# Optimization experiments

Hardware: AMD Instinct MI355X
Metric: run time of the kernel (lower is better)

Reference implementation:

```python
import jax, jax.numpy as jnp
import numpy as np

B, T, D, NH = 2, 2048, 2048, 16
HID = D  # hidden_dim must equal emb_dim for the source's fc2(x1) to type-check
HD = D // NH
EPS = 1e-5


def setup_inputs() -> dict:
    key = jax.random.key(0)
    ks = jax.random.split(key, 16)
    s = 0.02
    inp = {
        "x": jax.random.normal(ks[0], (B, T, D), jnp.float32),
        "Wq": jax.random.normal(ks[1], (D, D), jnp.float32) * s,
        "bq": jnp.zeros((D,), jnp.float32),
        "Wk": jax.random.normal(ks[2], (D, D), jnp.float32) * s,
        "bk": jnp.zeros((D,), jnp.float32),
        "Wv": jax.random.normal(ks[3], (D, D), jnp.float32) * s,
        "bv": jnp.zeros((D,), jnp.float32),
        "Wo": jax.random.normal(ks[4], (D, D), jnp.float32) * s,
        "bo": jnp.zeros((D,), jnp.float32),
        "scale1": jnp.ones((D,), jnp.float32),
        "scale2": jnp.ones((D,), jnp.float32),
        "W1": jax.random.normal(ks[5], (D, HID), jnp.float32) * s,
        "W2": jax.random.normal(ks[6], (D, HID), jnp.float32) * s,  # fc2: Linear(emb_dim, hidden_dim)
        "W3": jax.random.normal(ks[7], (HID, D), jnp.float32) * s,
    }
    return inp


def _rmsnorm(x, scale):
    m = jnp.mean(x * x, axis=-1, keepdims=True)
    return scale * (x * jax.lax.rsqrt(m + EPS))


def _attention(x, Wq, bq, Wk, bk, Wv, bv, Wo, bo):
    b, t, _ = x.shape
    q = (x @ Wq + bq).reshape(b, t, NH, HD)
    k = (x @ Wk + bk).reshape(b, t, NH, HD)
    v = (x @ Wv + bv).reshape(b, t, NH, HD)
    # energy: [B, H, T, T]; softmax over keys, scaled by 1/sqrt(head_dim); NO causal mask in source
    energy = jnp.einsum("bqhd,bkhd->bhqk", q, k) / jnp.sqrt(jnp.float32(HD))
    attn = jax.nn.softmax(energy, axis=-1)
    out = jnp.einsum("bhqk,bkhd->bqhd", attn, v).reshape(b, t, D)
    return out @ Wo + bo


def _ffn(x, W1, W2, W3):
    x1 = x @ W1                       # [B,T,HID]
    x2 = x1 @ W2                      # source quirk: fc2 applied to x1 (hidden_dim == emb_dim)
    return (x1 * jax.nn.sigmoid(x1) * x2) @ W3


def reference(x, Wq, bq, Wk, bk, Wv, bv, Wo, bo, scale1, scale2, W1, W2, W3):
    shortcut = x
    h = _rmsnorm(x, scale1)
    h = _attention(h, Wq, bq, Wk, bk, Wv, bv, Wo, bo)
    h = shortcut + h
    h = _rmsnorm(h, scale2)
    h = _ffn(h, W1, W2, W3)
    # source adds the ORIGINAL input again (shortcut never reassigned)
    return h + shortcut
```

## Files before the change

kernel.cpp:

```cpp
#include <hip/hip_runtime.h>

typedef __bf16 bf16x8 __attribute__((ext_vector_type(8)));
typedef __bf16 bf16x4v __attribute__((ext_vector_type(4)));
typedef float  f32x4  __attribute__((ext_vector_type(4)));

#define LDS_AS(p) ((__attribute__((address_space(3))) void*)(p))
#define GLB_AS(p) ((const __attribute__((address_space(1))) void*)(p))

#define QSCL (0.08838834764831845f * 1.4426950408889634f)

struct TP { const float* s[7]; __bf16* d[7]; float sc[7]; };
__global__ __launch_bounds__(256) void transpose_convert_all(TP p) {
  const float* __restrict__ W = p.s[blockIdx.z];
  __bf16* __restrict__ Wt = p.d[blockIdx.z];
  const float sc = p.sc[blockIdx.z];
  __shared__ float tile[32][33];
  const int tx = threadIdx.x & 31, ty = threadIdx.x >> 5;
  const int n0 = blockIdx.x * 32, k0 = blockIdx.y * 32;
#pragma unroll
  for (int j = 0; j < 4; ++j)
    tile[ty + j * 8][tx] = W[(size_t)(k0 + ty + j * 8) * 2048 + n0 + tx];
  __syncthreads();
#pragma unroll
  for (int j = 0; j < 4; ++j)
    Wt[(size_t)(n0 + ty + j * 8) * 2048 + k0 + tx] = (__bf16)(tile[tx][ty + j * 8] * sc);
}

__global__ __launch_bounds__(256) void rmsnorm_k(
    const float* __restrict__ x, const float* __restrict__ scale,
    __bf16* __restrict__ out) {
  const int row = blockIdx.x, t = threadIdx.x;
  const float4* xr = (const float4*)(x + (size_t)row * 2048);
  float4 a = xr[t], b2 = xr[t + 256];
  float ss = a.x * a.x + a.y * a.y + a.z * a.z + a.w * a.w +
             b2.x * b2.x + b2.y * b2.y + b2.z * b2.z + b2.w * b2.w;
#pragma unroll
  for (int ofs = 32; ofs; ofs >>= 1) ss += __shfl_xor(ss, ofs, 64);
  __shared__ float red[4];
  if ((t & 63) == 0) red[t >> 6] = ss;
  __syncthreads();
  ss = red[0] + red[1] + red[2] + red[3];
  const float rs = rsqrtf(ss * (1.f / 2048.f) + 1e-5f);
  const float4* sr = (const float4*)scale;
  float4 s1 = sr[t], s2 = sr[t + 256];
  __bf16* orow = out + (size_t)row * 2048;
  orow[t * 4 + 0] = (__bf16)(a.x * rs * s1.x);
  orow[t * 4 + 1] = (__bf16)(a.y * rs * s1.y);
  orow[t * 4 + 2] = (__bf16)(a.z * rs * s1.z);
  orow[t * 4 + 3] = (__bf16)(a.w * rs * s1.w);
  orow[(t + 256) * 4 + 0] = (__bf16)(b2.x * rs * s2.x);
  orow[(t + 256) * 4 + 1] = (__bf16)(b2.y * rs * s2.y);
  orow[(t + 256) * 4 + 2] = (__bf16)(b2.z * rs * s2.z);
  orow[(t + 256) * 4 + 3] = (__bf16)(b2.w * rs * s2.w);
}

template <bool OUTF32, bool HASBIAS, bool HASRES, bool SILU, bool VTRANS = false>
__global__ __launch_bounds__(256) void gemm_bt(
    const __bf16* __restrict__ A, const __bf16* __restrict__ Bt,
    const float* __restrict__ bias, const float* __restrict__ res,
    const __bf16* __restrict__ ew, void* __restrict__ Cout,
    int M, int N, int Kd) {
  __shared__ __attribute__((aligned(16))) __bf16 As[2][128 * 32];
  __shared__ __attribute__((aligned(16))) __bf16 Bs[2][128 * 32];
  const int tid = threadIdx.x;
  const int w = tid >> 6, l = tid & 63;
  const int flat = blockIdx.y * gridDim.x + blockIdx.x;
  const int nwg = gridDim.x * gridDim.y;
  const int swz = (flat & 7) * (nwg >> 3) + (flat >> 3);
  const int bx = swz % gridDim.x, by = swz / gridDim.x;
  const int M0 = by * 128, N0 = bx * 128;
  const int wr = w >> 1, wc = w & 1;
  const int lm = l & 15, lq = l >> 4;

  f32x4 acc[4][4];
#pragma unroll
  for (int mt = 0; mt < 4; ++mt)
#pragma unroll
    for (int nt = 0; nt < 4; ++nt)
#pragma unroll
      for (int e = 0; e < 4; ++e) acc[mt][nt][e] = 0.f;

  const int offA0 = (w * 2 + 0) * 1024 + l * 16;
  const int offA1 = (w * 2 + 1) * 1024 + l * 16;
  const int row0 = offA0 >> 6, kb0 = offA0 & 63;
  const int row1 = offA1 >> 6, kb1 = offA1 & 63;
  const int nIt = Kd >> 5;

  auto stage = [&](int k0, int bsel) {
    const char* ga0 = (const char*)(A + (size_t)(M0 + row0) * Kd + k0) + kb0;
    const char* ga1 = (const char*)(A + (size_t)(M0 + row1) * Kd + k0) + kb1;
    const char* gb0 = (const char*)(Bt + (size_t)(N0 + row0) * Kd + k0) + kb0;
    const char* gb1 = (const char*)(Bt + (size_t)(N0 + row1) * Kd + k0) + kb1;
    __builtin_amdgcn_global_load_lds(GLB_AS(ga0), LDS_AS(((char*)As[bsel]) + (w * 2 + 0) * 1024), 16, 0, 0);
    __builtin_amdgcn_global_load_lds(GLB_AS(ga1), LDS_AS(((char*)As[bsel]) + (w * 2 + 1) * 1024), 16, 0, 0);
    __builtin_amdgcn_global_load_lds(GLB_AS(gb0), LDS_AS(((char*)Bs[bsel]) + (w * 2 + 0) * 1024), 16, 0, 0);
    __builtin_amdgcn_global_load_lds(GLB_AS(gb1), LDS_AS(((char*)Bs[bsel]) + (w * 2 + 1) * 1024), 16, 0, 0);
  };

  stage(0, 0);
  for (int it = 0; it < nIt; ++it) {
    __syncthreads();
    if (it + 1 < nIt) stage((it + 1) * 32, (it + 1) & 1);
    const __bf16* Ab = As[it & 1];
    const __bf16* Bb = Bs[it & 1];
    bf16x8 af[4], bfr[4];
#pragma unroll
    for (int mt = 0; mt < 4; ++mt)
      af[mt] = *(const bf16x8*)(Ab + (wr * 64 + mt * 16 + lm) * 32 + lq * 8);
#pragma unroll
    for (int nt = 0; nt < 4; ++nt)
      bfr[nt] = *(const bf16x8*)(Bb + (wc * 64 + nt * 16 + lm) * 32 + lq * 8);
#pragma unroll
    for (int mt = 0; mt < 4; ++mt)
#pragma unroll
      for (int nt = 0; nt < 4; ++nt)
        acc[mt][nt] = __builtin_amdgcn_mfma_f32_16x16x32_bf16(af[mt], bfr[nt], acc[mt][nt], 0, 0, 0);
  }

  const int lr = lq * 4;
#pragma unroll
  for (int mt = 0; mt < 4; ++mt) {
#pragma unroll
    for (int nt = 0; nt < 4; ++nt) {
      const int col = N0 + wc * 64 + nt * 16 + lm;
      float bv = 0.f;
      if (HASBIAS) bv = bias[col];
      if (VTRANS) {
        const int rw0 = M0 + wr * 64 + mt * 16 + lr;
        const int bidx = rw0 >> 11, tok = rw0 & 2047;
        bf16x4v pk;
#pragma unroll
        for (int i = 0; i < 4; ++i) pk[i] = (__bf16)(acc[mt][nt][i] + bv);
        *(bf16x4v*)((__bf16*)Cout + ((size_t)(bidx * 2048 + col)) * 2048 + tok) = pk;
      } else {
#pragma unroll
        for (int i = 0; i < 4; ++i) {
          const int row = M0 + wr * 64 + mt * 16 + lr + i;
          const size_t off = (size_t)row * N + col;
          float v = acc[mt][nt][i] + bv;
          if (HASRES) v += res[off];
          if (SILU) {
            const float x1v = (float)ew[off];
            v = x1v * (1.f / (1.f + __expf(-x1v))) * v;
          }
          if (OUTF32) ((float*)Cout)[off] = v;
          else ((__bf16*)Cout)[off] = (__bf16)v;
        }
      }
    }
  }
}

__global__ __launch_bounds__(512, 2) void gemm_qkv(
    const __bf16* __restrict__ A, const __bf16* __restrict__ Bt,
    const float* __restrict__ bq, const float* __restrict__ bk,
    __bf16* __restrict__ Qout, __bf16* __restrict__ Kout, int Kd) {
  __shared__ __attribute__((aligned(16))) char lds[2][4][16384];

  const int tid = threadIdx.x;
  const int w = tid >> 6, l = tid & 63;
  const int wr = w >> 2, wc = w & 3;
  const int lm = l & 15, lq = l >> 4;

  const int flat = blockIdx.y * 16 + blockIdx.x;
  const int swz = (flat & 7) * 32 + (flat >> 3);
  const int bx = swz >> 4, by = swz & 15;
  const int N0 = bx * 256, M0 = by * 256;

  const int srow = w * 8 + (l >> 3);
  const int scol = ((l & 7) ^ (l >> 3)) * 8;
  const __bf16* aS = A + (size_t)(M0 + srow) * Kd + scol;
  const __bf16* bS = Bt + (size_t)(N0 + srow) * Kd + scol;

  auto stageHT = [&](int t, int s, int db) {
    char* dst = lds[db][s] + w * 1024;
    const __bf16* src = (s >= 2) ? (aS + (size_t)(s - 2) * 128 * Kd + t * 64)
                                 : (bS + (size_t)s * 128 * Kd + t * 64);
    __builtin_amdgcn_global_load_lds(GLB_AS(src), LDS_AS(dst), 16, 0, 0);
    __builtin_amdgcn_global_load_lds(GLB_AS(src + (size_t)64 * Kd), LDS_AS(dst + 8192), 16, 0, 0);
  };

  f32x4 acc[8][4];
#pragma unroll
  for (int m = 0; m < 8; ++m)
#pragma unroll
    for (int n = 0; n < 4; ++n)
#pragma unroll
      for (int e = 0; e < 4; ++e) acc[m][n][e] = 0.f;

  const int swzr = (lm & 7) << 4;
  const int c0 = (lq * 16) ^ swzr;
  const int c1 = ((64 + lq * 16)) ^ swzr;
  const int arow = lm * 128;
  const int brow = ((wc & 1) * 64 + lm) * 128;

  stageHT(0, 0, 0); stageHT(0, 1, 0); stageHT(0, 2, 0); stageHT(0, 3, 0);
  stageHT(1, 0, 1); stageHT(1, 1, 1); stageHT(1, 2, 1);
  asm volatile("s_waitcnt vmcnt(6)" ::: "memory");
  __builtin_amdgcn_s_barrier();

  const int NT = Kd >> 6;
  bf16x8 af[4][2], bfr[4][2];

#define BAR()                                            \
  do {                                                   \
    asm volatile("" ::: "memory");                       \
    __builtin_amdgcn_s_barrier();                        \
    asm volatile("" ::: "memory");                       \
  } while (0)

#define MFMA_QUAD(MB, NB)                                                          \
  do {                                                                             \
    _Pragma("unroll") for (int m = 0; m < 4; ++m)                                  \
      _Pragma("unroll") for (int n = 0; n < 2; ++n) {                              \
        acc[(MB) + m][(NB) + n] = __builtin_amdgcn_mfma_f32_16x16x32_bf16(         \
            af[m][0], bfr[(NB) + n][0], acc[(MB) + m][(NB) + n], 0, 0, 0);         \
        acc[(MB) + m][(NB) + n] = __builtin_amdgcn_mfma_f32_16x16x32_bf16(         \
            af[m][1], bfr[(NB) + n][1], acc[(MB) + m][(NB) + n], 0, 0, 0);         \
      }                                                                            \
  } while (0)

#define TILE_BODY(T, BUF)                                                       \
  do {                                                                          \
    const char* Ab = lds[BUF][2 + wr];                                          \
    const char* Bb = lds[BUF][wc >> 1];                                         \
    _Pragma("unroll") for (int m = 0; m < 4; ++m) {                             \
      af[m][0] = *(const bf16x8*)(Ab + arow + m * 2048 + c0);                   \
      af[m][1] = *(const bf16x8*)(Ab + arow + m * 2048 + c1);                   \
    }                                                                           \
    _Pragma("unroll") for (int n = 0; n < 4; ++n) {                             \
      bfr[n][0] = *(const bf16x8*)(Bb + brow + n * 2048 + c0);                  \
      bfr[n][1] = *(const bf16x8*)(Bb + brow + n * 2048 + c1);                  \
    }                                                                           \
    if ((T) + 1 < NT) stageHT((T) + 1, 3, (BUF) ^ 1);                           \
    BAR();                                                                      \
    __builtin_amdgcn_s_setprio(1);                                              \
    MFMA_QUAD(0, 0);                                                            \
    __builtin_amdgcn_s_setprio(0);                                              \
    asm volatile("s_waitcnt lgkmcnt(0)" ::: "memory");                          \
    BAR();                                                                      \
    if ((T) + 2 < NT) stageHT((T) + 2, 0, BUF);                                 \
    BAR();                                                                      \
    __builtin_amdgcn_s_setprio(1);                                              \
    MFMA_QUAD(0, 2);                                                            \
    __builtin_amdgcn_s_setprio(0);                                              \
    BAR();                                                                      \
    _Pragma("unroll") for (int m = 0; m < 4; ++m) {                             \
      af[m][0] = *(const bf16x8*)(Ab + arow + (m + 4) * 2048 + c0);             \
      af[m][1] = *(const bf16x8*)(Ab + arow + (m + 4) * 2048 + c1);             \
    }                                                                           \
    if ((T) + 2 < NT) stageHT((T) + 2, 1, BUF);                                 \
    BAR();                                                                      \
    __builtin_amdgcn_s_setprio(1);                                              \
    MFMA_QUAD(4, 0);                                                            \
    __builtin_amdgcn_s_setprio(0);                                              \
    asm volatile("s_waitcnt lgkmcnt(0)" ::: "memory");                          \
    BAR();                                                                      \
    if ((T) + 2 < NT) stageHT((T) + 2, 2, BUF);                                 \
    BAR();                                                                      \
    __builtin_amdgcn_s_setprio(1);                                              \
    MFMA_QUAD(4, 2);                                                            \
    __builtin_amdgcn_s_setprio(0);                                              \
    if ((T) + 2 < NT) { asm volatile("s_waitcnt vmcnt(6)" ::: "memory"); }      \
    else { asm volatile("s_waitcnt vmcnt(0)" ::: "memory"); }                   \
    BAR();                                                                      \
  } while (0)

  for (int tp = 0; tp < NT; tp += 2) {
    TILE_BODY(tp, 0);
    TILE_BODY(tp + 1, 1);
  }
#undef TILE_BODY
#undef MFMA_QUAD
#undef BAR

  const int seg = N0 >> 11;
  const int nbase = N0 & 2047;
  const float* bb = (seg == 0) ? bq : bk;
  const float bsc = (seg == 0) ? QSCL : 1.f;
  __bf16* dst = (seg == 0) ? Qout : Kout;
#pragma unroll
  for (int m = 0; m < 8; ++m) {
#pragma unroll
    for (int n = 0; n < 4; ++n) {
      const int col = nbase + wc * 64 + n * 16 + lm;
      const float bvv = bb[col] * bsc;
#pragma unroll
      for (int i = 0; i < 4; ++i) {
        const int row = M0 + wr * 128 + m * 16 + lq * 4 + i;
        dst[(size_t)row * 2048 + col] = (__bf16)(acc[m][n][i] + bvv);
      }
    }
  }
}

__global__ __launch_bounds__(256, 2) void attn_mfma(
    const __bf16* __restrict__ Q, const __bf16* __restrict__ K,
    const __bf16* __restrict__ Vt, __bf16* __restrict__ O) {
  __shared__ __attribute__((aligned(16))) char KsL[2][16 * 1024];
  __shared__ __attribute__((aligned(16))) char VsL[2][16 * 1024];

  const int t = threadIdx.x;
  const int w = t >> 6, l = t & 63;
  const int lm = l & 15, quad = l >> 4;
  const int flat = (blockIdx.z * gridDim.y + blockIdx.y) * gridDim.x + blockIdx.x;
  const int swz = (flat & 7) * 64 + (flat >> 3);
  const int b = swz >> 8;
  const int h = (swz >> 4) & 15;
  const int q0 = (swz & 15) * 128;
  const size_t Ds = 2048;
  const size_t hoff = (size_t)h * 128;
  const size_t bbase = (size_t)b * 2048;
  const int slq = (lm << 2) | quad;
  const int sl16 = (slq ^ ((slq >> 3) & 7)) * 16;

  const int slog = l ^ ((l >> 3) & 7);
  const int krow = slog >> 2, kcol = (slog & 3) * 8;
  const int vth = l & 3, vd = l >> 2;

  bf16x8 onesv;
#pragma unroll
  for (int i = 0; i < 8; ++i) onesv[i] = (__bf16)1.0f;

  bf16x8 qf[2][4];
#pragma unroll
  for (int ntq = 0; ntq < 2; ++ntq)
#pragma unroll
    for (int ks = 0; ks < 4; ++ks)
      qf[ntq][ks] = *(const bf16x8*)(Q + (bbase + q0 + w * 32 + ntq * 16 + lm) * Ds + hoff + ks * 32 + quad * 8);

  f32x4 oacc[2][8];
#pragma unroll
  for (int ntq = 0; ntq < 2; ++ntq)
#pragma unroll
    for (int nv = 0; nv < 8; ++nv)
#pragma unroll
      for (int e = 0; e < 4; ++e) oacc[ntq][nv][e] = 0.f;
  f32x4 lacc[2];
#pragma unroll
  for (int ntq = 0; ntq < 2; ++ntq)
#pragma unroll
    for (int e = 0; e < 4; ++e) lacc[ntq][e] = 0.f;

  bf16x8 vreg[4];

  auto loadV = [&](int kt) {
#pragma unroll
    for (int i = 0; i < 4; ++i) {
      const int chunk = w * 4 + i;
      const int nv = chunk >> 1, c = chunk & 1;
      vreg[i] = *(const bf16x8*)(Vt + (bbase + hoff + nv * 16 + vd) * Ds + kt + c * 32 + vth * 8);
    }
  };
  auto stageK = [&](int kt, char* Kb) {
#pragma unroll
    for (int i = 0; i < 4; ++i) {
      const __bf16* src = K + (bbase + kt + i * 16 + krow) * Ds + hoff + w * 32 + kcol;
      __builtin_amdgcn_global_load_lds(GLB_AS(src), LDS_AS(Kb + (i * 4 + w) * 1024), 16, 0, 0);
    }
  };
  auto writeV = [&](char* Vb) {
    const int slot_a = (vd << 2) | ((vth & 1) << 1);
    const int o_a = (slot_a ^ ((vd >> 1) & 7)) * 16 + (vth >> 1) * 8;
#pragma unroll
    for (int i = 0; i < 4; ++i) {
      char* base = Vb + (w * 4 + i) * 1024;
      uint4 u = *(const uint4*)&vreg[i];
      *(uint2*)(base + o_a) = make_uint2(u.x, u.y);
      *(uint2*)(base + (o_a ^ 16)) = make_uint2(u.z, u.w);
    }
  };

  loadV(0);
  stageK(0, KsL[0]);
  writeV(VsL[0]);

  for (int it = 0; it < 32; ++it) {
    __syncthreads();
    const int cur = it & 1;
    const bool more = (it + 1) < 32;
    if (more) { loadV((it + 1) * 64); stageK((it + 1) * 64, KsL[(it + 1) & 1]); }

    const char* Kb = KsL[cur];
    const char* Vb = VsL[cur];

    f32x4 st[4][2];
#pragma unroll
    for (int mtk = 0; mtk < 4; ++mtk)
#pragma unroll
      for (int ntq = 0; ntq < 2; ++ntq)
#pragma unroll
        for (int e = 0; e < 4; ++e) st[mtk][ntq][e] = 0.f;
    __builtin_amdgcn_s_setprio(1);
#pragma unroll
    for (int ks = 0; ks < 4; ++ks) {
#pragma unroll
      for (int mtk = 0; mtk < 4; ++mtk) {
        bf16x8 kf = *(const bf16x8*)(Kb + (mtk * 4 + ks) * 1024 + sl16);
        st[mtk][0] = __builtin_amdgcn_mfma_f32_16x16x32_bf16(kf, qf[0][ks], st[mtk][0], 0, 0, 0);
        st[mtk][1] = __builtin_amdgcn_mfma_f32_16x16x32_bf16(kf, qf[1][ks], st[mtk][1], 0, 0, 0);
      }
    }
    __builtin_amdgcn_s_setprio(0);

#pragma unroll
    for (int c = 0; c < 2; ++c) {
      bf16x8 pf[2];
#pragma unroll
      for (int ntq = 0; ntq < 2; ++ntq) {
#pragma unroll
        for (int half = 0; half < 2; ++half) {
          const f32x4 sv = st[c * 2 + half][ntq];
#pragma unroll
          for (int r = 0; r < 4; ++r)
            pf[ntq][half * 4 + r] = (__bf16)exp2f(sv[r]);
        }
      }
      __builtin_amdgcn_s_setprio(1);
      lacc[0] = __builtin_amdgcn_mfma_f32_16x16x32_bf16(pf[0], onesv, lacc[0], 0, 0, 0);
      lacc[1] = __builtin_amdgcn_mfma_f32_16x16x32_bf16(pf[1], onesv, lacc[1], 0, 0, 0);
#pragma unroll
      for (int nv = 0; nv < 8; ++nv) {
        bf16x8 vf = *(const bf16x8*)(Vb + (nv * 2 + c) * 1024 + sl16);
        oacc[0][nv] = __builtin_amdgcn_mfma_f32_16x16x32_bf16(pf[0], vf, oacc[0][nv], 0, 0, 0);
        oacc[1][nv] = __builtin_amdgcn_mfma_f32_16x16x32_bf16(pf[1], vf, oacc[1][nv], 0, 0, 0);
      }
      __builtin_amdgcn_s_setprio(0);
    }

    if (more) writeV(VsL[(it + 1) & 1]);
  }

  float oinv[2][4];
#pragma unroll
  for (int ntq = 0; ntq < 2; ++ntq)
#pragma unroll
    for (int r = 0; r < 4; ++r)
      oinv[ntq][r] = 1.f / lacc[ntq][r];

#pragma unroll
  for (int ntq = 0; ntq < 2; ++ntq)
#pragma unroll
    for (int nv = 0; nv < 8; ++nv)
#pragma unroll
      for (int r = 0; r < 4; ++r) {
        const int qrow = q0 + w * 32 + ntq * 16 + quad * 4 + r;
        O[(bbase + qrow) * Ds + hoff + nv * 16 + lm] = (__bf16)(oacc[ntq][nv][r] * oinv[ntq][r]);
      }
}

extern "C" void kernel_launch(void* const* d_in, const int* in_sizes, int n_in,
                              void* d_out, int out_size, void* d_ws, size_t ws_size,
                              hipStream_t stream) {
  const float* x      = (const float*)d_in[0];
  const float* Wq     = (const float*)d_in[1];
  const float* bq     = (const float*)d_in[2];
  const float* Wk     = (const float*)d_in[3];
  const float* bk     = (const float*)d_in[4];
  const float* Wv     = (const float*)d_in[5];
  const float* bv     = (const float*)d_in[6];
  const float* Wo     = (const float*)d_in[7];
  const float* bo     = (const float*)d_in[8];
  const float* scale1 = (const float*)d_in[9];
  const float* scale2 = (const float*)d_in[10];
  const float* W1     = (const float*)d_in[11];
  const float* W2     = (const float*)d_in[12];
  const float* W3     = (const float*)d_in[13];

  const int M = 4096, N = 2048, Kd = 2048;
  char* ws = (char*)d_ws;
  const size_t WT_B = (size_t)2048 * 2048 * 2;
  const size_t ACT_B = (size_t)4096 * 2048 * 2;
  __bf16* wt[7];
  size_t off = 0;
  for (int i = 0; i < 7; ++i) { wt[i] = (__bf16*)(ws + off); off += WT_B; }
  __bf16* hn1  = (__bf16*)(ws + off); off += ACT_B;
  __bf16* Qb   = (__bf16*)(ws + off); off += ACT_B;
  __bf16* Kb   = (__bf16*)(ws + off); off += ACT_B;
  __bf16* VtG  = (__bf16*)(ws + off); off += ACT_B;
  __bf16* attn = (__bf16*)(ws + off); off += ACT_B;
  __bf16* hn2  = (__bf16*)(ws + off); off += ACT_B;
  __bf16* x1b  = (__bf16*)(ws + off); off += ACT_B;
  __bf16* fmb  = (__bf16*)(ws + off); off += ACT_B;

  dim3 tb(256);
  {
    TP p;
    p.s[0] = Wq; p.s[1] = Wk; p.s[2] = Wv; p.s[3] = Wo; p.s[4] = W1; p.s[5] = W2; p.s[6] = W3;
    for (int i = 0; i < 7; ++i) { p.d[i] = wt[i]; p.sc[i] = 1.f; }
    p.sc[0] = QSCL;
    transpose_convert_all<<<dim3(64, 64, 7), tb, 0, stream>>>(p);
  }

  rmsnorm_k<<<4096, tb, 0, stream>>>(x, scale1, hn1);

  gemm_qkv<<<dim3(16, 16), dim3(512), 0, stream>>>(hn1, wt[0], bq, bk, Qb, Kb, Kd);
  gemm_bt<false, true, false, false, true><<<dim3(16, 32), tb, 0, stream>>>(
      hn1, wt[2], bv, nullptr, nullptr, VtG, M, 2048, Kd);

  dim3 ag(2048 / 128, 16, 2);
  attn_mfma<<<ag, tb, 0, stream>>>(Qb, Kb, VtG, attn);

  dim3 gg(N / 128, M / 128);
  gemm_bt<true, true, true, false><<<gg, tb, 0, stream>>>(attn, wt[3], bo, x, nullptr, d_out, M, N, Kd);

  rmsnorm_k<<<4096, tb, 0, stream>>>((const float*)d_out, scale2, hn2);

  gemm_bt<false, false, false, false><<<gg, tb, 0, stream>>>(hn2, wt[4], nullptr, nullptr, nullptr, x1b, M, N, Kd);
  gemm_bt<false, false, false, true><<<gg, tb, 0, stream>>>(x1b, wt[5], nullptr, nullptr, x1b, fmb, M, N, Kd);
  gemm_bt<true, false, true, false><<<gg, tb, 0, stream>>>(fmb, wt[6], nullptr, x, nullptr, d_out, M, N, Kd);
}
```

Baseline: 603.0 us.

## Replace generic bf16 GEMM with 256x128 tile, 8-wave, swizzled, interleaved-prefetch kernel

Replaces the 128x128, 256-thread double-buffered GEMM with a 512-thread kernel computing 256x128 tiles at K-step 64. It uses XOR-swizzled LDS layouts and staged global->LDS loads split into half-tiles, interleaved with MFMA quads under barriers and s_setprio. The aim is to hide memory latency, avoid LDS bank conflicts and raise MFMA density for the V, output-projection and FFN GEMMs. The grid indexing is hardcoded to 16x16 blocks (M=4096, N=2048), and the more complex barrier schedule risks stalls.

```diff
diff --git a/kernel.cpp b/kernel.cpp
--- a/kernel.cpp
+++ b/kernel.cpp
@@ -54,70 +54,128 @@
   orow[(t + 256) * 4 + 3] = (__bf16)(b2.w * rs * s2.w);
 }
 
-template <bool OUTF32, bool HASBIAS, bool HASRES, bool SILU, bool VTRANS = false>
-__global__ __launch_bounds__(256) void gemm_bt(
+template <bool OUTF32, bool HASBIAS, bool HASRES, bool SILU, bool VTRANS>
+__global__ __launch_bounds__(512, 2) void gemm_bt2(
     const __bf16* __restrict__ A, const __bf16* __restrict__ Bt,
     const float* __restrict__ bias, const float* __restrict__ res,
     const __bf16* __restrict__ ew, void* __restrict__ Cout,
     int M, int N, int Kd) {
-  __shared__ __attribute__((aligned(16))) __bf16 As[2][128 * 32];
-  __shared__ __attribute__((aligned(16))) __bf16 Bs[2][128 * 32];
+  __shared__ __attribute__((aligned(16))) char lds[2][3][16384];
+
   const int tid = threadIdx.x;
   const int w = tid >> 6, l = tid & 63;
-  const int flat = blockIdx.y * gridDim.x + blockIdx.x;
-  const int nwg = gridDim.x * gridDim.y;
-  const int swz = (flat & 7) * (nwg >> 3) + (flat >> 3);
-  const int bx = swz % gridDim.x, by = swz / gridDim.x;
-  const int M0 = by * 128, N0 = bx * 128;
   const int wr = w >> 1, wc = w & 1;
   const int lm = l & 15, lq = l >> 4;
 
+  const int flat = blockIdx.y * 16 + blockIdx.x;
+  const int swz = (flat & 7) * 32 + (flat >> 3);
+  const int bx = swz >> 4, by = swz & 15;
+  const int N0 = bx * 128, M0 = by * 256;
+
+  const int srow = w * 8 + (l >> 3);
+  const int scol = ((l & 7) ^ (l >> 3)) * 8;
+  const __bf16* aS = A + (size_t)(M0 + srow) * Kd + scol;
+  const __bf16* bS = Bt + (size_t)(N0 + srow) * Kd + scol;
+
+  auto stageHT = [&](int t, int s, int db) {
+    char* dst = lds[db][s] + w * 1024;
+    const __bf16* src = (s == 0) ? (bS + t * 64)
+                                 : (aS + (size_t)(s - 1) * 128 * Kd + t * 64);
+    __builtin_amdgcn_global_load_lds(GLB_AS(src), LDS_AS(dst), 16, 0, 0);
+    __builtin_amdgcn_global_load_lds(GLB_AS(src + (size_t)64 * Kd), LDS_AS(dst + 8192), 16, 0, 0);
+  };
+
   f32x4 acc[4][4];
 #pragma unroll
-  for (int mt = 0; mt < 4; ++mt)
-#pragma unroll
-    for (int nt = 0; nt < 4; ++nt)
-#pragma unroll
-      for (int e = 0; e < 4; ++e) acc[mt][nt][e] = 0.f;
-
-  const int offA0 = (w * 2 + 0) * 1024 + l * 16;
-  const int offA1 = (w * 2 + 1) * 1024 + l * 16;
-  const int row0 = offA0 >> 6, kb0 = offA0 & 63;
-  const int row1 = offA1 >> 6, kb1 = offA1 & 63;
-  const int nIt = Kd >> 5;
-
-  auto stage = [&](int k0, int bsel) {
-    const char* ga0 = (const char*)(A + (size_t)(M0 + row0) * Kd + k0) + kb0;
-    const char* ga1 = (const char*)(A + (size_t)(M0 + row1) * Kd + k0) + kb1;
-    const char* gb0 = (const char*)(Bt + (size_t)(N0 + row0) * Kd + k0) + kb0;
-    const char* gb1 = (const char*)(Bt + (size_t)(N0 + row1) * Kd + k0) + kb1;
-    __builtin_amdgcn_global_load_lds(GLB_AS(ga0), LDS_AS(((char*)As[bsel]) + (w * 2 + 0) * 1024), 16, 0, 0);
-    __builtin_amdgcn_global_load_lds(GLB_AS(ga1), LDS_AS(((char*)As[bsel]) + (w * 2 + 1) * 1024), 16, 0, 0);
-    __builtin_amdgcn_global_load_lds(GLB_AS(gb0), LDS_AS(((char*)Bs[bsel]) + (w * 2 + 0) * 1024), 16, 0, 0);
-    __builtin_amdgcn_global_load_lds(GLB_AS(gb1), LDS_AS(((char*)Bs[bsel]) + (w * 2 + 1) * 1024), 16, 0, 0);
-  };
-
-  stage(0, 0);
-  for (int it = 0; it < nIt; ++it) {
-    __syncthreads();
-    if (it + 1 < nIt) stage((it + 1) * 32, (it + 1) & 1);
-    const __bf16* Ab = As[it & 1];
-    const __bf16* Bb = Bs[it & 1];
-    bf16x8 af[4], bfr[4];
-#pragma unroll
-    for (int mt = 0; mt < 4; ++mt)
-      af[mt] = *(const bf16x8*)(Ab + (wr * 64 + mt * 16 + lm) * 32 + lq * 8);
-#pragma unroll
-    for (int nt = 0; nt < 4; ++nt)
-      bfr[nt] = *(const bf16x8*)(Bb + (wc * 64 + nt * 16 + lm) * 32 + lq * 8);
-#pragma unroll
-    for (int mt = 0; mt < 4; ++mt)
-#pragma unroll
-      for (int nt = 0; nt < 4; ++nt)
-        acc[mt][nt] = __builtin_amdgcn_mfma_f32_16x16x32_bf16(af[mt], bfr[nt], acc[mt][nt], 0, 0, 0);
+  for (int m = 0; m < 4; ++m)
+#pragma unroll
+    for (int n = 0; n < 4; ++n)
+#pragma unroll
+      for (int e = 0; e < 4; ++e) acc[m][n][e] = 0.f;
+
+  const int swzr = (lm & 7) << 4;
+  const int c0 = (lq * 16) ^ swzr;
+  const int c1 = ((64 + lq * 16)) ^ swzr;
+  const int arow = (wr & 1) * 8192 + lm * 128;
+  const int brow = wc * 8192 + lm * 128;
+
+  stageHT(0, 0, 0); stageHT(0, 1, 0); stageHT(0, 2, 0);
+  stageHT(1, 0, 1); stageHT(1, 1, 1);
+  asm volatile("s_waitcnt vmcnt(4)" ::: "memory");
+  __builtin_amdgcn_s_barrier();
+
+  const int NT = Kd >> 6;
+  bf16x8 af[4][2], bfr[4][2];
+
+#define BAR()                                            \
+  do {                                                   \
+    asm volatile("" ::: "memory");                       \
+    __builtin_amdgcn_s_barrier();                        \
+    asm volatile("" ::: "memory");                       \
+  } while (0)
+
+#define MFMA_QUAD(MB, NB)                                                          \
+  do {                                                                             \
+    _Pragma("unroll") for (int m = 0; m < 2; ++m)                                  \
+      _Pragma("unroll") for (int n = 0; n < 2; ++n) {                              \
+        acc[(MB) + m][(NB) + n] = __builtin_amdgcn_mfma_f32_16x16x32_bf16(         \
+            af[(MB) + m][0], bfr[(NB) + n][0], acc[(MB) + m][(NB) + n], 0, 0, 0);  \
+        acc[(MB) + m][(NB) + n] = __builtin_amdgcn_mfma_f32_16x16x32_bf16(         \
+            af[(MB) + m][1], bfr[(NB) + n][1], acc[(MB) + m][(NB) + n], 0, 0, 0);  \
+      }                                                                            \
+  } while (0)
+
+#define TILE_BODY(T, BUF)                                                       \
+  do {                                                                          \
+    const char* Ab = lds[BUF][1 + (wr >> 1)];                                   \
+    const char* Bb = lds[BUF][0];                                               \
+         \
+    _Pragma("unroll") for (int m = 0; m < 4; ++m) {                             \
+      af[m][0] = *(const bf16x8*)(Ab + arow + m * 2048 + c0);                   \
+      af[m][1] = *(const bf16x8*)(Ab + arow + m * 2048 + c1);                   \
+    }                                                                           \
+    _Pragma("unroll") for (int n = 0; n < 4; ++n) {                             \
+      bfr[n][0] = *(const bf16x8*)(Bb + brow + n * 2048 + c0);                  \
+      bfr[n][1] = *(const bf16x8*)(Bb + brow + n * 2048 + c1);                  \
+    }                                                                           \
+    if ((T) + 1 < NT) stageHT((T) + 1, 2, (BUF) ^ 1);                           \
+    BAR();                                                                      \
+    __builtin_amdgcn_s_setprio(1);                                              \
+    MFMA_QUAD(0, 0);                                                            \
+    __builtin_amdgcn_s_setprio(0);                                              \
+    asm volatile("s_waitcnt lgkmcnt(0)" ::: "memory");                          \
+    BAR();                                                                      \
+                                          \
+    if ((T) + 2 < NT) stageHT((T) + 2, 0, BUF);                                 \
+    BAR();                                                                      \
+    __builtin_amdgcn_s_setprio(1);                                              \
+    MFMA_QUAD(0, 2);                                                            \
+    __builtin_amdgcn_s_setprio(0);                                              \
+    BAR();                                                                      \
+                                          \
+    if ((T) + 2 < NT) stageHT((T) + 2, 1, BUF);                                 \
+    BAR();                                                                      \
+    __builtin_amdgcn_s_setprio(1);                                              \
+    MFMA_QUAD(2, 0);                                                            \
+    __builtin_amdgcn_s_setprio(0);                                              \
+    BAR();                                                                      \
+                                             \
+    __builtin_amdgcn_s_setprio(1);                                              \
+    MFMA_QUAD(2, 2);                                                            \
+    __builtin_amdgcn_s_setprio(0);                                              \
+    if ((T) + 2 < NT) { asm volatile("s_waitcnt vmcnt(4)" ::: "memory"); }      \
+    else { asm volatile("s_waitcnt vmcnt(0)" ::: "memory"); }                   \
+    BAR();                                                                      \
+  } while (0)
+
+  for (int tp = 0; tp < NT; tp += 2) {
+    TILE_BODY(tp, 0);
+    TILE_BODY(tp + 1, 1);
   }
-
-  const int lr = lq * 4;
+#undef TILE_BODY
+#undef MFMA_QUAD
+#undef BAR
+
 #pragma unroll
   for (int mt = 0; mt < 4; ++mt) {
 #pragma unroll
@@ -126,7 +184,7 @@
       float bv = 0.f;
       if (HASBIAS) bv = bias[col];
       if (VTRANS) {
-        const int rw0 = M0 + wr * 64 + mt * 16 + lr;
+        const int rw0 = M0 + wr * 64 + mt * 16 + lq * 4;
         const int bidx = rw0 >> 11, tok = rw0 & 2047;
         bf16x4v pk;
 #pragma unroll
@@ -135,7 +193,7 @@
       } else {
 #pragma unroll
         for (int i = 0; i < 4; ++i) {
-          const int row = M0 + wr * 64 + mt * 16 + lr + i;
+          const int row = M0 + wr * 64 + mt * 16 + lq * 4 + i;
           const size_t off = (size_t)row * N + col;
           float v = acc[mt][nt][i] + bv;
           if (HASRES) v += res[off];
@@ -495,18 +553,22 @@
   rmsnorm_k<<<4096, tb, 0, stream>>>(x, scale1, hn1);
 
   gemm_qkv<<<dim3(16, 16), dim3(512), 0, stream>>>(hn1, wt[0], bq, bk, Qb, Kb, Kd);
-  gemm_bt<false, true, false, false, true><<<dim3(16, 32), tb, 0, stream>>>(
+  gemm_bt2<false, true, false, false, true><<<dim3(16, 16), dim3(512), 0, stream>>>(
       hn1, wt[2], bv, nullptr, nullptr, VtG, M, 2048, Kd);
 
   dim3 ag(2048 / 128, 16, 2);
   attn_mfma<<<ag, tb, 0, stream>>>(Qb, Kb, VtG, attn);
 
-  dim3 gg(N / 128, M / 128);
-  gemm_bt<true, true, true, false><<<gg, tb, 0, stream>>>(attn, wt[3], bo, x, nullptr, d_out, M, N, Kd);
+  dim3 gg2(16, 16);
+  gemm_bt2<true, true, true, false, false><<<gg2, dim3(512), 0, stream>>>(
+      attn, wt[3], bo, x, nullptr, d_out, M, N, Kd);
 
   rmsnorm_k<<<4096, tb, 0, stream>>>((const float*)d_out, scale2, hn2);
 
-  gemm_bt<false, false, false, false><<<gg, tb, 0, stream>>>(hn2, wt[4], nullptr, nullptr, nullptr, x1b, M, N, Kd);
-  gemm_bt<false, false, false, true><<<gg, tb, 0, stream>>>(x1b, wt[5], nullptr, nullptr, x1b, fmb, M, N, Kd);
-  gemm_bt<true, false, true, false><<<gg, tb, 0, stream>>>(fmb, wt[6], nullptr, x, nullptr, d_out, M, N, Kd);
+  gemm_bt2<false, false, false, false, false><<<gg2, dim3(512), 0, stream>>>(
+      hn2, wt[4], nullptr, nullptr, nullptr, x1b, M, N, Kd);
+  gemm_bt2<false, false, false, true, false><<<gg2, dim3(512), 0, stream>>>(
+      x1b, wt[5], nullptr, nullptr, x1b, fmb, M, N, Kd);
+  gemm_bt2<true, false, true, false, false><<<gg2, dim3(512), 0, stream>>>(
+      fmb, wt[6], nullptr, x, nullptr, d_out, M, N, Kd);
 }
```

Result: faster. 561.0 us (-7.0%).
